# Performance work log

Measured on AMD Instinct MI355X. Metric: run time of the kernel, lower is better.

## Reference

```python
import jax, jax.numpy as jnp
import numpy as np

B, N, C, H = 32, 512, 1024, 16
HD = C // H  # head_dim = 64
SCALE = HD ** -0.5


def setup_inputs() -> dict:
    key = jax.random.key(0)
    k1, k2, k3, k4 = jax.random.split(key, 4)
    # xavier_uniform bounds
    qkv_bound = (6.0 / (C + 3 * C)) ** 0.5
    proj_bound = 1.414 * (6.0 / (C + C)) ** 0.5
    return {
        "x": jax.random.normal(k1, (B, N, C), dtype=jnp.float32),
        "mask": jax.random.uniform(k2, (B, N), dtype=jnp.float32),
        "W_qkv": jax.random.uniform(k3, (3 * C, C), dtype=jnp.float32, minval=-qkv_bound, maxval=qkv_bound),
        "W_proj": jax.random.uniform(k4, (C, C), dtype=jnp.float32, minval=-proj_bound, maxval=proj_bound),
        "b_proj": jnp.zeros((C,), dtype=jnp.float32),
    }


def reference(x, mask, W_qkv, W_proj, b_proj):
    # qkv projection (no bias): [B,N,3C] -> [3,B,H,N,HD]
    qkv = jnp.einsum("bnc,dc->bnd", x, W_qkv)
    qkv = qkv.reshape(B, N, 3, H, HD).transpose(2, 0, 3, 1, 4)
    q, k, v = qkv[0] * SCALE, qkv[1], qkv[2]
    # attention scores [B,H,N,N] with additive row/col mask bias
    attn = jnp.einsum("bhqd,bhkd->bhqk", q, k)
    attn = attn + mask[:, None, None, :] + mask[:, None, :, None]
    attn = jax.nn.softmax(attn, axis=-1)
    out = jnp.einsum("bhqk,bhkd->bhqd", attn, v)
    out = out.transpose(0, 2, 1, 3).reshape(B, N, C)
    return jnp.einsum("bnc,dc->bnd", out, W_proj) + b_proj
```

## Files before the change

### kernel.cpp

```cpp
#include <hip/hip_runtime.h>
#include <stdint.h>

typedef unsigned short u16;
typedef __bf16 bf16x8 __attribute__((ext_vector_type(8)));
typedef float  f32x4  __attribute__((ext_vector_type(4)));
typedef float  f32x16 __attribute__((ext_vector_type(16)));
typedef unsigned int u32x4 __attribute__((ext_vector_type(4)));

#define MFMA16(a,b,c) __builtin_amdgcn_mfma_f32_16x16x32_bf16((a),(b),(c),0,0,0)
#define MFMA32(a,b,c) __builtin_amdgcn_mfma_f32_32x32x16_bf16((a),(b),(c),0,0,0)

#if __has_builtin(__builtin_amdgcn_exp2f)
#define EXP2F(x) __builtin_amdgcn_exp2f(x)
#else
#define EXP2F(x) exp2f(x)
#endif

__device__ __forceinline__ u16 f2b(float f) {
  unsigned int u = __builtin_bit_cast(unsigned int, f);
  u += 0x7fffu + ((u >> 16) & 1u);
  return (u16)(u >> 16);
}

__device__ __forceinline__ void gll16(const u16* g, u16* l) {
  __builtin_amdgcn_global_load_lds((const __attribute__((address_space(1))) unsigned int*)g,
                                   (__attribute__((address_space(3))) unsigned int*)l,
                                   16, 0, 0);
}

__device__ __forceinline__ unsigned cvtpk(float lo, float hi) {
  unsigned r;
  asm("v_cvt_pk_bf16_f32 %0, %1, %2" : "=v"(r) : "v"(lo), "v"(hi));
  return r;
}
__device__ __forceinline__ void pl32swap(unsigned &x, unsigned &y) {
  asm volatile("v_permlane32_swap_b32 %0, %1" : "+v"(x), "+v"(y));
}

#define BARR() __builtin_amdgcn_s_barrier()
#define SCHED0() __builtin_amdgcn_sched_barrier(0)
#define LGKM(N) do { asm volatile("s_waitcnt lgkmcnt(" #N ")" ::: "memory"); __builtin_amdgcn_sched_barrier(0); } while (0)
#define VMC(N) do { asm volatile("s_waitcnt vmcnt(" #N ")" ::: "memory"); __builtin_amdgcn_sched_barrier(0); } while (0)
#define PRIO1() __builtin_amdgcn_s_setprio(1)
#define PRIO0() __builtin_amdgcn_s_setprio(0)

__global__ __launch_bounds__(256)
void cvt_all(const float* __restrict__ X, const float* __restrict__ Wq,
             const float* __restrict__ Wp, u16* __restrict__ Xb,
             u16* __restrict__ Wqb, u16* __restrict__ Wpb)
{
  size_t i = (size_t)blockIdx.x * 256 + threadIdx.x;
  const float* src; u16* dst; size_t off;
  if (i < 4194304)       { src = X;  dst = Xb;  off = i; }
  else if (i < 4980736)  { src = Wq; dst = Wqb; off = i - 4194304; }
  else                   { src = Wp; dst = Wpb; off = i - 4980736; }
  float4 v = ((const float4*)src)[off];
  uint2 p;
  p.x = f2b(v.x) | ((unsigned)f2b(v.y) << 16);
  p.y = f2b(v.z) | ((unsigned)f2b(v.w) << 16);
  ((uint2*)dst)[off] = p;
}

#define DS_A(CUR, AF, RBASE) do { \
  _Pragma("unroll") for (int mt = 0; mt < 4; mt++) \
  _Pragma("unroll") for (int ks = 0; ks < 2; ks++) \
    AF[mt][ks] = *(const bf16x8*)((const char*)Asmem[CUR] + (RBASE) + aoff[mt][ks]); \
} while (0)

#define DS_B2(CUR, N0) do { \
  _Pragma("unroll") for (int nt = 0; nt < 2; nt++) \
  _Pragma("unroll") for (int ks = 0; ks < 2; ks++) \
    bfr[(N0) + nt][ks] = *(const bf16x8*)((const char*)Bsmem[CUR] + boff[(N0) + nt][ks]); \
} while (0)

#define MQ(MB, NB, AF) do { \
  _Pragma("unroll") for (int mt = 0; mt < 4; mt++) \
  _Pragma("unroll") for (int nt = 0; nt < 2; nt++) \
  _Pragma("unroll") for (int ks = 0; ks < 2; ks++) \
    acc[(MB) + mt][(NB) + nt] = MFMA16(AF[mt][ks], bfr[(NB) + nt][ks], acc[(MB) + mt][(NB) + nt]); \
} while (0)

#define HALF_ITER(CUR, TA, TB, ENDW) do { \
   \
  DS_A(CUR, afl, 0); DS_B2(CUR, 0); SCHED0(); \
  DS_B2(CUR, 2); SCHED0(); \
  DS_A(CUR, afh, 8192); SCHED0(); \
  STAGE_A(TA, 0); STAGE_A(TA, 1); \
  LGKM(12); PRIO1(); MQ(0, 0, afl); PRIO0(); \
  LGKM(8);  PRIO1(); MQ(0, 2, afl); PRIO0(); \
  BARR();   \
  STAGE_B(TB, 0); STAGE_B(TB, 1); \
  LGKM(0);  PRIO1(); MQ(4, 0, afh); MQ(4, 2, afh); PRIO0(); \
  ENDW; \
  BARR(); \
} while (0)

template <int EPI>
__global__ __launch_bounds__(512, 2)
void gemm8p(const u16* __restrict__ Ag, const u16* __restrict__ Wg,
            u16* __restrict__ qb, u16* __restrict__ kb, u16* __restrict__ vT,
            const float* __restrict__ bias, float* __restrict__ outf, int nbx)
{
  __shared__ u16 Asmem[2][16384];
  __shared__ u16 Bsmem[2][16384];

  const int nwg = gridDim.x;
  const int cpx = nwg >> 3;
  const int bid = blockIdx.x;
  const int wg  = (bid & 7) * cpx + (bid >> 3);
  const int bx = wg % nbx, by = wg / nbx;
  const int row0 = by * 256, col0 = bx * 256;

  const int t = threadIdx.x;
  const int lane = t & 63, w = t >> 6;
  const int quad = lane >> 4, l16 = lane & 15;
  const int wm = w >> 2, wn = w & 3;
  const int sx = l16 & 7;

  const int srow = lane >> 3;
  const int scol = ((lane & 7) ^ srow) * 8;
  const u16* pA0 = Ag + (size_t)(row0 + w * 16 + srow) * 1024 + scol;
  const u16* pB0 = Wg + (size_t)(col0 + w * 16 + srow) * 1024 + scol;

  int aoff[4][2], boff[4][2];
#pragma unroll
  for (int mt = 0; mt < 4; mt++)
#pragma unroll
    for (int ks = 0; ks < 2; ks++) {
      int r = wm * 128 + mt * 16 + l16;
      aoff[mt][ks] = r * 128 + (((ks * 4 + quad) ^ sx) * 16);
    }
#pragma unroll
  for (int nt = 0; nt < 4; nt++)
#pragma unroll
    for (int ks = 0; ks < 2; ks++) {
      int r = wn * 64 + nt * 16 + l16;
      boff[nt][ks] = r * 128 + (((ks * 4 + quad) ^ sx) * 16);
    }

  f32x4 acc[8][4];
#pragma unroll
  for (int i = 0; i < 8; i++)
#pragma unroll
    for (int j = 0; j < 4; j++) acc[i][j] = f32x4{0.f, 0.f, 0.f, 0.f};

  auto STAGE_A = [&](int tile, int half) {
    if (tile >= 16) return;
    const u16* g = pA0 + (size_t)half * 131072 + tile * 64;
    u16* l = &Asmem[tile & 1][(half * 128 + w * 16) * 64];
    gll16(g, l);
    gll16(g + 8192, l + 512);
  };
  auto STAGE_B = [&](int tile, int half) {
    if (tile >= 16) return;
    const u16* g = pB0 + (size_t)half * 131072 + tile * 64;
    u16* l = &Bsmem[tile & 1][(half * 128 + w * 16) * 64];
    gll16(g, l);
    gll16(g + 8192, l + 512);
  };

  bf16x8 afl[4][2], afh[4][2], bfr[4][2];

  STAGE_B(0, 0); STAGE_B(0, 1); STAGE_A(0, 0); STAGE_A(0, 1);
  SCHED0();
  STAGE_B(1, 0); STAGE_B(1, 1);
  VMC(4); BARR();

#pragma unroll 1
  for (int i = 0; i < 7; ++i) {
    int t1 = 2 * i + 1;
    HALF_ITER(0, t1, t1 + 1, VMC(4));
    HALF_ITER(1, t1 + 1, t1 + 2, VMC(4));
  }
  HALF_ITER(0, 15, 16, VMC(0));
  HALF_ITER(1, 16, 17, ((void)0));

  const int tok_base = row0 + wm * 128;
  if constexpr (EPI == 0) {
#pragma unroll
    for (int nt = 0; nt < 4; nt++) {
      int d = col0 + wn * 64 + nt * 16;
      int part = d >> 10;
      int hh = (d >> 6) & 15;
      int hd = (d & 63) + l16;
      if (part == 2) {
#pragma unroll
        for (int mt = 0; mt < 8; mt++) {
          int nb = tok_base + mt * 16 + quad * 4;
          int bb = nb >> 9, nn = nb & 511;
          uint2 pk;
          pk.x = f2b(acc[mt][nt][0]) | ((unsigned)f2b(acc[mt][nt][1]) << 16);
          pk.y = f2b(acc[mt][nt][2]) | ((unsigned)f2b(acc[mt][nt][3]) << 16);
          *(uint2*)(vT + (((size_t)(bb * 16 + hh)) * 64 + hd) * 512 + nn) = pk;
        }
      } else {
        u16* dst = (part == 0) ? qb : kb;
        float sc = (part == 0) ? 0.125f : 1.0f;
#pragma unroll
        for (int mt = 0; mt < 8; mt++)
#pragma unroll
          for (int r = 0; r < 4; r++) {
            int tok = tok_base + mt * 16 + quad * 4 + r;
            int bb = tok >> 9, nn = tok & 511;
            dst[(((size_t)(bb * 16 + hh)) * 512 + nn) * 64 + hd] = f2b(acc[mt][nt][r] * sc);
          }
      }
    }
  } else {
#pragma unroll
    for (int nt = 0; nt < 4; nt++) {
      int d = col0 + wn * 64 + nt * 16 + l16;
      float bv = bias[d];
#pragma unroll
      for (int mt = 0; mt < 8; mt++)
#pragma unroll
        for (int r = 0; r < 4; r++) {
          int tok = tok_base + mt * 16 + quad * 4 + r;
          outf[(size_t)tok * 1024 + d] = acc[mt][nt][r] + bv;
        }
    }
  }
}

__global__ __launch_bounds__(256)
void attn_kernel(const u16* __restrict__ qb, const u16* __restrict__ kb,
                 const u16* __restrict__ vT, const float* __restrict__ mask,
                 u16* __restrict__ ao)
{
  __shared__ u16 Kbuf[2][64 * 64];
  __shared__ u16 Vbuf[2][64 * 64];
  __shared__ float mk2[512];
  __shared__ float Lbuf[128];

  const int bid = blockIdx.x;
  const int wid = (bid & 7) * 256 + (bid >> 3);
  const int qt = wid & 3, bh = wid >> 2;
  const int b = bh >> 4, hh = bh & 15;

  const int t = threadIdx.x;
  const int lane = t & 63, w = t >> 6;
  const int l31 = lane & 31, hi = lane >> 5;
  const int sw = l31 & 7;

  const u16* Qp = qb + (size_t)bh * 512 * 64;
  const u16* Kp = kb + (size_t)bh * 512 * 64;
  const u16* Vp = vT + (size_t)bh * 64 * 512;

  for (int i = t; i < 512; i += 256) mk2[i] = mask[b * 512 + i] * 1.44269504f;

  const int qbase = qt * 128 + w * 32;
  bf16x8 qf[4];
#pragma unroll
  for (int dc = 0; dc < 4; dc++)
    qf[dc] = *(const bf16x8*)(Qp + (size_t)(qbase + l31) * 64 + dc * 16 + hi * 8);

  const int sr = lane >> 3, sc = lane & 7;
  const int cg = sc ^ sr;
  const u16* gk[2]; const u16* gv[2];
#pragma unroll
  for (int j = 0; j < 2; j++) {
    int r = w * 16 + j * 8 + sr;
    gk[j] = Kp + (size_t)r * 64 + cg * 8;
    gv[j] = Vp + (size_t)r * 512 + cg * 8;
  }

  f32x16 oacc[2];
#pragma unroll
  for (int i = 0; i < 16; i++) { oacc[0][i] = 0.f; oacc[1][i] = 0.f; }
  float lsum = 0.f;

  auto STAGE = [&](int tt, int buf) {
#pragma unroll
    for (int j = 0; j < 2; j++) {
      gll16(gk[j] + (size_t)tt * 4096, &Kbuf[buf][(w * 16 + j * 8) * 64]);
      gll16(gv[j] + (size_t)tt * 64,   &Vbuf[buf][(w * 16 + j * 8) * 64]);
    }
  };

  STAGE(0, 0);
  __syncthreads();

  for (int tt = 0; tt < 8; tt++) {
    const int cur = tt & 1;
    if (tt < 7) STAGE(tt + 1, cur ^ 1);
    const u16* Kb = Kbuf[cur];
    const u16* Vb = Vbuf[cur];
#pragma unroll
    for (int c = 0; c < 2; c++) {
      f32x16 s;
#pragma unroll
      for (int i = 0; i < 16; i++) s[i] = 0.f;
#pragma unroll
      for (int dc = 0; dc < 4; dc++) {
        int row = c * 32 + l31;
        bf16x8 kf = *(const bf16x8*)((const char*)Kb + row * 128 + (((2 * dc + hi) ^ sw) * 16));
        s = MFMA32(kf, qf[dc], s);
      }
      const int kb0 = tt * 64 + c * 32;
      f32x4 mkv[4];
#pragma unroll
      for (int g = 0; g < 4; g++) mkv[g] = *(const f32x4*)(mk2 + kb0 + g * 8 + hi * 4);
      float p[16];
#pragma unroll
      for (int r = 0; r < 16; r++)
        p[r] = EXP2F(fmaf(s[r], 1.44269504f, mkv[r >> 2][r & 3]));
      float ls = 0.f;
#pragma unroll
      for (int r = 0; r < 16; r++) ls += p[r];
      lsum += ls;

      unsigned d0a = cvtpk(p[0],  p[1]),  d1a = cvtpk(p[2],  p[3]);
      unsigned d2a = cvtpk(p[4],  p[5]),  d3a = cvtpk(p[6],  p[7]);
      unsigned d0b = cvtpk(p[8],  p[9]),  d1b = cvtpk(p[10], p[11]);
      unsigned d2b = cvtpk(p[12], p[13]), d3b = cvtpk(p[14], p[15]);
      pl32swap(d0a, d2a);
      pl32swap(d1a, d3a);
      pl32swap(d0b, d2b);
      pl32swap(d1b, d3b);
      u32x4 w0; w0.x = d0a; w0.y = d1a; w0.z = d2a; w0.w = d3a;
      u32x4 w1; w1.x = d0b; w1.y = d1b; w1.z = d2b; w1.w = d3b;
      bf16x8 af[2];
      af[0] = __builtin_bit_cast(bf16x8, w0);
      af[1] = __builtin_bit_cast(bf16x8, w1);

#pragma unroll
      for (int kc = 0; kc < 2; kc++)
#pragma unroll
        for (int dc = 0; dc < 2; dc++) {
          int row = dc * 32 + l31;
          bf16x8 vf = *(const bf16x8*)((const char*)Vb + row * 128 + (((4 * c + 2 * kc + hi) ^ sw) * 16));
          oacc[dc] = MFMA32(af[kc], vf, oacc[dc]);
        }
    }
    __syncthreads();
  }

  lsum += __shfl_xor(lsum, 32);
  if (lane < 32) Lbuf[w * 32 + l31] = 1.0f / lsum;
  __syncthreads();
  f32x4 inv4[4];
#pragma unroll
  for (int g = 0; g < 4; g++) inv4[g] = *(const f32x4*)(Lbuf + w * 32 + g * 8 + hi * 4);

#pragma unroll
  for (int dc = 0; dc < 2; dc++)
#pragma unroll
    for (int r = 0; r < 16; r++) {
      int qrow = (r & 3) + 8 * (r >> 2) + 4 * hi;
      int n = qbase + qrow;
      int col = hh * 64 + dc * 32 + l31;
      ao[((size_t)(b * 512 + n)) * 1024 + col] = f2b(oacc[dc][r] * inv4[r >> 2][r & 3]);
    }
}

extern "C" void kernel_launch(void* const* d_in, const int* in_sizes, int n_in,
                              void* d_out, int out_size, void* d_ws, size_t ws_size,
                              hipStream_t stream) {
  const float* x     = (const float*)d_in[0];
  const float* mask  = (const float*)d_in[1];
  const float* Wqkv  = (const float*)d_in[2];
  const float* Wproj = (const float*)d_in[3];
  const float* bproj = (const float*)d_in[4];
  float* out = (float*)d_out;

  u16* qb  = (u16*)d_ws;
  u16* kb  = qb + 16777216;
  u16* vT  = kb + 16777216;
  u16* XbAo = vT + 16777216;
  u16* Wqb = XbAo + 16777216;
  u16* Wpb = Wqb + 3145728;

  cvt_all<<<20480, 256, 0, stream>>>(x, Wqkv, Wproj, XbAo, Wqb, Wpb);
  gemm8p<0><<<768, 512, 0, stream>>>(XbAo, Wqb, qb, kb, vT, nullptr, nullptr, 12);
  attn_kernel<<<2048, 256, 0, stream>>>(qb, kb, vT, mask, XbAo);
  gemm8p<1><<<256, 512, 0, stream>>>(XbAo, Wpb, nullptr, nullptr, nullptr, bproj, out, 4);
}
```

Before: 331.2 us.

## Triple-buffer A tiles in GEMM to prefetch two tiles ahead

Grows the A shared-memory staging from two buffers to three and rewrites the main loop as a six-step rotation, so A tiles are fetched two iterations ahead while B stays double-buffered. Wait counts are raised to allow more outstanding global loads. The aim is to hide global load latency in the QKV and projection GEMMs. The cost is 32KB more LDS per block, 160KB in total at two blocks per CU, and a more complex buffer-index schedule that must stay consistent.

After: 376.1 us. 1.14x slower.

```diff
diff --git a/kernel.cpp b/kernel.cpp
--- a/kernel.cpp
+++ b/kernel.cpp
@@ -80,16 +80,15 @@
     acc[(MB) + mt][(NB) + nt] = MFMA16(AF[mt][ks], bfr[(NB) + nt][ks], acc[(MB) + mt][(NB) + nt]); \
 } while (0)
 
-#define HALF_ITER(CUR, TA, TB, ENDW) do { \
-   \
-  DS_A(CUR, afl, 0); DS_B2(CUR, 0); SCHED0(); \
-  DS_B2(CUR, 2); SCHED0(); \
-  DS_A(CUR, afh, 8192); SCHED0(); \
-  STAGE_A(TA, 0); STAGE_A(TA, 1); \
+#define HALF_ITER(CA, NA, CB, TA, TB, ENDW) do { \
+  DS_A(CA, afl, 0); DS_B2(CB, 0); SCHED0(); \
+  DS_B2(CB, 2); SCHED0(); \
+  DS_A(CA, afh, 8192); SCHED0(); \
+  STAGE_A(TA, 0, NA); STAGE_A(TA, 1, NA); \
   LGKM(12); PRIO1(); MQ(0, 0, afl); PRIO0(); \
   LGKM(8);  PRIO1(); MQ(0, 2, afl); PRIO0(); \
   BARR();   \
-  STAGE_B(TB, 0); STAGE_B(TB, 1); \
+  STAGE_B(TB, 0, CB); STAGE_B(TB, 1, CB); \
   LGKM(0);  PRIO1(); MQ(4, 0, afh); MQ(4, 2, afh); PRIO0(); \
   ENDW; \
   BARR(); \
@@ -101,7 +100,7 @@
             u16* __restrict__ qb, u16* __restrict__ kb, u16* __restrict__ vT,
             const float* __restrict__ bias, float* __restrict__ outf, int nbx)
 {
-  __shared__ u16 Asmem[2][16384];
+  __shared__ u16 Asmem[3][16384];
   __shared__ u16 Bsmem[2][16384];
 
   const int nwg = gridDim.x;
@@ -144,36 +143,42 @@
 #pragma unroll
     for (int j = 0; j < 4; j++) acc[i][j] = f32x4{0.f, 0.f, 0.f, 0.f};
 
-  auto STAGE_A = [&](int tile, int half) {
+  auto STAGE_A = [&](int tile, int half, int dst) {
     if (tile >= 16) return;
     const u16* g = pA0 + (size_t)half * 131072 + tile * 64;
-    u16* l = &Asmem[tile & 1][(half * 128 + w * 16) * 64];
+    u16* l = &Asmem[dst][(half * 128 + w * 16) * 64];
     gll16(g, l);
     gll16(g + 8192, l + 512);
   };
-  auto STAGE_B = [&](int tile, int half) {
+  auto STAGE_B = [&](int tile, int half, int dst) {
     if (tile >= 16) return;
     const u16* g = pB0 + (size_t)half * 131072 + tile * 64;
-    u16* l = &Bsmem[tile & 1][(half * 128 + w * 16) * 64];
+    u16* l = &Bsmem[dst][(half * 128 + w * 16) * 64];
     gll16(g, l);
     gll16(g + 8192, l + 512);
   };
 
   bf16x8 afl[4][2], afh[4][2], bfr[4][2];
 
-  STAGE_B(0, 0); STAGE_B(0, 1); STAGE_A(0, 0); STAGE_A(0, 1);
+  STAGE_B(0, 0, 0); STAGE_B(0, 1, 0); STAGE_A(0, 0, 0); STAGE_A(0, 1, 0);
   SCHED0();
-  STAGE_B(1, 0); STAGE_B(1, 1);
-  VMC(4); BARR();
+  STAGE_B(1, 0, 1); STAGE_B(1, 1, 1); STAGE_A(1, 0, 1); STAGE_A(1, 1, 1);
+  VMC(8); BARR();
 
 #pragma unroll 1
-  for (int i = 0; i < 7; ++i) {
-    int t1 = 2 * i + 1;
-    HALF_ITER(0, t1, t1 + 1, VMC(4));
-    HALF_ITER(1, t1 + 1, t1 + 2, VMC(4));
+  for (int i = 0; i < 2; ++i) {
+    int T = 6 * i;
+    HALF_ITER(0, 2, 0, T + 2, T + 2, VMC(8));
+    HALF_ITER(1, 0, 1, T + 3, T + 3, VMC(8));
+    HALF_ITER(2, 1, 0, T + 4, T + 4, VMC(8));
+    HALF_ITER(0, 2, 1, T + 5, T + 5, VMC(8));
+    HALF_ITER(1, 0, 0, T + 6, T + 6, VMC(8));
+    HALF_ITER(2, 1, 1, T + 7, T + 7, VMC(8));
   }
-  HALF_ITER(0, 15, 16, VMC(0));
-  HALF_ITER(1, 16, 17, ((void)0));
+  HALF_ITER(0, 2, 0, 14, 14, VMC(8));
+  HALF_ITER(1, 0, 1, 15, 15, VMC(8));
+  HALF_ITER(2, 1, 0, 16, 16, VMC(0));
+  HALF_ITER(0, 2, 1, 17, 17, ((void)0));
 
   const int tok_base = row0 + wm * 128;
   if constexpr (EPI == 0) {
```

## Process two 32-row query groups per wave in attention to reuse K/V tiles

Applied to the files above, without the earlier changes.

Each attention wave now handles 64 query rows as two 32-row groups instead of one, so every block covers 256 queries and the grid shrinks from 2048 to 1024 blocks. Each K and V fragment read from shared memory feeds two MFMAs, and the global staging of K and V per query row is halved. The cost is roughly double the accumulator and probability registers per thread and fewer blocks in flight, with launch bounds set to ask for two blocks per CU.

New measurement: 326.4 us. No clear change (-1.4%).

```diff
diff --git a/kernel.cpp b/kernel.cpp
--- a/kernel.cpp
+++ b/kernel.cpp
@@ -81,7 +81,6 @@
 } while (0)
 
 #define HALF_ITER(CUR, TA, TB, ENDW) do { \
-   \
   DS_A(CUR, afl, 0); DS_B2(CUR, 0); SCHED0(); \
   DS_B2(CUR, 2); SCHED0(); \
   DS_A(CUR, afh, 8192); SCHED0(); \
@@ -222,7 +221,7 @@
   }
 }
 
-__global__ __launch_bounds__(256)
+__global__ __launch_bounds__(256, 2)
 void attn_kernel(const u16* __restrict__ qb, const u16* __restrict__ kb,
                  const u16* __restrict__ vT, const float* __restrict__ mask,
                  u16* __restrict__ ao)
@@ -230,11 +229,11 @@
   __shared__ u16 Kbuf[2][64 * 64];
   __shared__ u16 Vbuf[2][64 * 64];
   __shared__ float mk2[512];
-  __shared__ float Lbuf[128];
+  __shared__ float Lbuf[256];
 
   const int bid = blockIdx.x;
-  const int wid = (bid & 7) * 256 + (bid >> 3);
-  const int qt = wid & 3, bh = wid >> 2;
+  const int wid = (bid & 7) * 128 + (bid >> 3);
+  const int qt = wid & 1, bh = wid >> 1;
   const int b = bh >> 4, hh = bh & 15;
 
   const int t = threadIdx.x;
@@ -248,11 +247,13 @@
 
   for (int i = t; i < 512; i += 256) mk2[i] = mask[b * 512 + i] * 1.44269504f;
 
-  const int qbase = qt * 128 + w * 32;
-  bf16x8 qf[4];
-#pragma unroll
-  for (int dc = 0; dc < 4; dc++)
-    qf[dc] = *(const bf16x8*)(Qp + (size_t)(qbase + l31) * 64 + dc * 16 + hi * 8);
+  const int qbase = qt * 256 + w * 64;
+  bf16x8 qf[2][4];
+#pragma unroll
+  for (int g = 0; g < 2; g++)
+#pragma unroll
+    for (int dc = 0; dc < 4; dc++)
+      qf[g][dc] = *(const bf16x8*)(Qp + (size_t)(qbase + g * 32 + l31) * 64 + dc * 16 + hi * 8);
 
   const int sr = lane >> 3, sc = lane & 7;
   const int cg = sc ^ sr;
@@ -264,10 +265,12 @@
     gv[j] = Vp + (size_t)r * 512 + cg * 8;
   }
 
-  f32x16 oacc[2];
-#pragma unroll
-  for (int i = 0; i < 16; i++) { oacc[0][i] = 0.f; oacc[1][i] = 0.f; }
-  float lsum = 0.f;
+  f32x16 oacc[2][2];
+#pragma unroll
+  for (int g = 0; g < 2; g++)
+#pragma unroll
+    for (int i = 0; i < 16; i++) { oacc[g][0][i] = 0.f; oacc[g][1][i] = 0.f; }
+  float lsum[2] = {0.f, 0.f};
 
   auto STAGE = [&](int tt, int buf) {
 #pragma unroll
@@ -287,41 +290,48 @@
     const u16* Vb = Vbuf[cur];
 #pragma unroll
     for (int c = 0; c < 2; c++) {
-      f32x16 s;
-#pragma unroll
-      for (int i = 0; i < 16; i++) s[i] = 0.f;
+      f32x16 s[2];
+#pragma unroll
+      for (int g = 0; g < 2; g++)
+#pragma unroll
+        for (int i = 0; i < 16; i++) s[g][i] = 0.f;
 #pragma unroll
       for (int dc = 0; dc < 4; dc++) {
         int row = c * 32 + l31;
         bf16x8 kf = *(const bf16x8*)((const char*)Kb + row * 128 + (((2 * dc + hi) ^ sw) * 16));
-        s = MFMA32(kf, qf[dc], s);
+        s[0] = MFMA32(kf, qf[0][dc], s[0]);
+        s[1] = MFMA32(kf, qf[1][dc], s[1]);
       }
       const int kb0 = tt * 64 + c * 32;
       f32x4 mkv[4];
 #pragma unroll
-      for (int g = 0; g < 4; g++) mkv[g] = *(const f32x4*)(mk2 + kb0 + g * 8 + hi * 4);
-      float p[16];
-#pragma unroll
-      for (int r = 0; r < 16; r++)
-        p[r] = EXP2F(fmaf(s[r], 1.44269504f, mkv[r >> 2][r & 3]));
-      float ls = 0.f;
-#pragma unroll
-      for (int r = 0; r < 16; r++) ls += p[r];
-      lsum += ls;
-
-      unsigned d0a = cvtpk(p[0],  p[1]),  d1a = cvtpk(p[2],  p[3]);
-      unsigned d2a = cvtpk(p[4],  p[5]),  d3a = cvtpk(p[6],  p[7]);
-      unsigned d0b = cvtpk(p[8],  p[9]),  d1b = cvtpk(p[10], p[11]);
-      unsigned d2b = cvtpk(p[12], p[13]), d3b = cvtpk(p[14], p[15]);
-      pl32swap(d0a, d2a);
-      pl32swap(d1a, d3a);
-      pl32swap(d0b, d2b);
-      pl32swap(d1b, d3b);
-      u32x4 w0; w0.x = d0a; w0.y = d1a; w0.z = d2a; w0.w = d3a;
-      u32x4 w1; w1.x = d0b; w1.y = d1b; w1.z = d2b; w1.w = d3b;
-      bf16x8 af[2];
-      af[0] = __builtin_bit_cast(bf16x8, w0);
-      af[1] = __builtin_bit_cast(bf16x8, w1);
+      for (int gg = 0; gg < 4; gg++) mkv[gg] = *(const f32x4*)(mk2 + kb0 + gg * 8 + hi * 4);
+
+      bf16x8 af[2][2];
+#pragma unroll
+      for (int g = 0; g < 2; g++) {
+        float p[16];
+#pragma unroll
+        for (int r = 0; r < 16; r++)
+          p[r] = EXP2F(fmaf(s[g][r], 1.44269504f, mkv[r >> 2][r & 3]));
+        float ls = 0.f;
+#pragma unroll
+        for (int r = 0; r < 16; r++) ls += p[r];
+        lsum[g] += ls;
+
+        unsigned d0a = cvtpk(p[0],  p[1]),  d1a = cvtpk(p[2],  p[3]);
+        unsigned d2a = cvtpk(p[4],  p[5]),  d3a = cvtpk(p[6],  p[7]);
+        unsigned d0b = cvtpk(p[8],  p[9]),  d1b = cvtpk(p[10], p[11]);
+        unsigned d2b = cvtpk(p[12], p[13]), d3b = cvtpk(p[14], p[15]);
+        pl32swap(d0a, d2a);
+        pl32swap(d1a, d3a);
+        pl32swap(d0b, d2b);
+        pl32swap(d1b, d3b);
+        u32x4 w0; w0.x = d0a; w0.y = d1a; w0.z = d2a; w0.w = d3a;
+        u32x4 w1; w1.x = d0b; w1.y = d1b; w1.z = d2b; w1.w = d3b;
+        af[g][0] = __builtin_bit_cast(bf16x8, w0);
+        af[g][1] = __builtin_bit_cast(bf16x8, w1);
+      }
 
 #pragma unroll
       for (int kc = 0; kc < 2; kc++)
@@ -329,28 +339,37 @@
         for (int dc = 0; dc < 2; dc++) {
           int row = dc * 32 + l31;
           bf16x8 vf = *(const bf16x8*)((const char*)Vb + row * 128 + (((4 * c + 2 * kc + hi) ^ sw) * 16));
-          oacc[dc] = MFMA32(af[kc], vf, oacc[dc]);
+          oacc[0][dc] = MFMA32(af[0][kc], vf, oacc[0][dc]);
+          oacc[1][dc] = MFMA32(af[1][kc], vf, oacc[1][dc]);
         }
     }
     __syncthreads();
   }
 
-  lsum += __shfl_xor(lsum, 32);
-  if (lane < 32) Lbuf[w * 32 + l31] = 1.0f / lsum;
+#pragma unroll
+  for (int g = 0; g < 2; g++) {
+    lsum[g] += __shfl_xor(lsum[g], 32);
+    if (lane < 32) Lbuf[w * 64 + g * 32 + l31] = 1.0f / lsum[g];
+  }
   __syncthreads();
-  f32x4 inv4[4];
-#pragma unroll
-  for (int g = 0; g < 4; g++) inv4[g] = *(const f32x4*)(Lbuf + w * 32 + g * 8 + hi * 4);
-
-#pragma unroll
-  for (int dc = 0; dc < 2; dc++)
-#pragma unroll
-    for (int r = 0; r < 16; r++) {
-      int qrow = (r & 3) + 8 * (r >> 2) + 4 * hi;
-      int n = qbase + qrow;
-      int col = hh * 64 + dc * 32 + l31;
-      ao[((size_t)(b * 512 + n)) * 1024 + col] = f2b(oacc[dc][r] * inv4[r >> 2][r & 3]);
-    }
+  f32x4 inv4[2][4];
+#pragma unroll
+  for (int g = 0; g < 2; g++)
+#pragma unroll
+    for (int gg = 0; gg < 4; gg++)
+      inv4[g][gg] = *(const f32x4*)(Lbuf + w * 64 + g * 32 + gg * 8 + hi * 4);
+
+#pragma unroll
+  for (int g = 0; g < 2; g++)
+#pragma unroll
+    for (int dc = 0; dc < 2; dc++)
+#pragma unroll
+      for (int r = 0; r < 16; r++) {
+        int qrow = (r & 3) + 8 * (r >> 2) + 4 * hi;
+        int n = qbase + g * 32 + qrow;
+        int col = hh * 64 + dc * 32 + l31;
+        ao[((size_t)(b * 512 + n)) * 1024 + col] = f2b(oacc[g][dc][r] * inv4[g][r >> 2][r & 3]);
+      }
 }
 
 extern "C" void kernel_launch(void* const* d_in, const int* in_sizes, int n_in,
@@ -372,6 +391,6 @@
 
   cvt_all<<<20480, 256, 0, stream>>>(x, Wqkv, Wproj, XbAo, Wqb, Wpb);
   gemm8p<0><<<768, 512, 0, stream>>>(XbAo, Wqb, qb, kb, vT, nullptr, nullptr, 12);
-  attn_kernel<<<2048, 256, 0, stream>>>(qb, kb, vT, mask, XbAo);
+  attn_kernel<<<1024, 256, 0, stream>>>(qb, kb, vT, mask, XbAo);
   gemm8p<1><<<256, 512, 0, stream>>>(XbAo, Wpb, nullptr, nullptr, nullptr, bproj, out, 4);
 }
```
